# Kernel tuning notes

Hardware: AMD Instinct MI355X
Metric: run time of the kernel (lower is better)

Reference implementation:

```python
import jax, jax.numpy as jnp
import numpy as np

B, N, C, HF, NUM_CLASS = 2, 500, 512, 25, 20
POOL = 7
STRIDE = 32.0


def setup_inputs() -> dict:
    key = jax.random.key(0)
    ks = jax.random.split(key, 9)
    feature_map = jax.random.normal(ks[0], (B, C, HF, HF), dtype=jnp.float32)
    # Post-NMS boxes (r0, c0, r1, c1) in image coords [0, 800], guaranteed
    # to have floor(r1/32) - floor(r0/32) >= 1 so every crop is non-empty
    # (matches the module's assumption that extract_fature_map is non-empty).
    r0 = jax.random.uniform(ks[1], (B, N), minval=0.0, maxval=700.0)
    c0 = jax.random.uniform(ks[2], (B, N), minval=0.0, maxval=700.0)
    hh = jax.random.uniform(ks[3], (B, N), minval=64.0, maxval=100.0)
    ww = jax.random.uniform(ks[4], (B, N), minval=64.0, maxval=100.0)
    boxes = jnp.stack([r0, c0, jnp.clip(r0 + hh, 0, 800.0), jnp.clip(c0 + ww, 0, 800.0)], axis=-1)
    fc_w = jax.random.normal(ks[5], (4096, POOL * POOL * C), dtype=jnp.float32) * 0.01
    fc_b = jnp.zeros((4096,), dtype=jnp.float32)
    l_w = jax.random.normal(ks[6], (NUM_CLASS * 4, 4096), dtype=jnp.float32) * 0.01
    l_b = jnp.zeros((NUM_CLASS * 4,), dtype=jnp.float32)
    s_w = jax.random.normal(ks[7], (NUM_CLASS + 1, 4096), dtype=jnp.float32) * 0.01
    s_b = jnp.zeros((NUM_CLASS + 1,), dtype=jnp.float32)
    return {"feature_map": feature_map, "boxes": boxes, "fc_w": fc_w, "fc_b": fc_b,
            "l_w": l_w, "l_b": l_b, "s_w": s_w, "s_b": s_b}


def _bin_edges(start, size):
    # Adaptive avg pool bin boundaries: floor(k*size/P), ceil((k+1)*size/P),
    # offset by the crop start. start/size: [B, N] int32. Returns [B, N, P] each.
    k = jnp.arange(POOL, dtype=jnp.int32)
    lo = start[..., None] + (k * size[..., None]) // POOL
    hi = start[..., None] + ((k + 1) * size[..., None] + POOL - 1) // POOL
    return lo, hi


def _roi_pool(feature_map, boxes):
    # Exact equivalent of per-box crop + AdaptiveAvgPool2d((7,7)) via an
    # integral image, fully vectorized over all B*N boxes.
    coords = (boxes / STRIDE).astype(jnp.int32)  # int() cast, coords >= 0
    r0, c0, r1, c1 = coords[..., 0], coords[..., 1], coords[..., 2], coords[..., 3]
    rs, re = _bin_edges(r0, r1 - r0)  # [B, N, 7]
    cs, ce = _bin_edges(c0, c1 - c0)
    # Integral image: I[b, ch, i, j] = sum(fm[b, ch, :i, :j]); shape [B, C, 26, 26]
    I = jnp.pad(feature_map, ((0, 0), (0, 0), (1, 0), (1, 0))).cumsum(2).cumsum(3)

    def pool_one(I_b, rs_b, re_b, cs_b, ce_b):
        def corner(r, c):  # [N,7],[N,7] -> [C, N, 7, 7]
            return I_b[:, r[:, :, None], c[:, None, :]]
        S = corner(re_b, ce_b) - corner(rs_b, ce_b) - corner(re_b, cs_b) + corner(rs_b, cs_b)
        area = ((re_b - rs_b)[:, :, None] * (ce_b - cs_b)[:, None, :]).astype(I_b.dtype)
        return S / area  # [C, N, 7, 7]

    pooled = jax.vmap(pool_one)(I, rs, re, cs, ce)  # [B, C, N, 7, 7]
    # torch.flatten(pool, 0) flattens (C, 7, 7) in C-major order
    return pooled.transpose(0, 2, 1, 3, 4).reshape(B, N, C * POOL * POOL)


def reference(feature_map, boxes, fc_w, fc_b, l_w, l_b, s_w, s_b):
    feat = _roi_pool(feature_map, boxes)                      # [B, N, 25088]
    fc = jnp.einsum('bnk,fk->bnf', feat, fc_w) + fc_b         # [B, N, 4096]
    l_fc = jnp.einsum('bnf,lf->bnl', fc, l_w) + l_b           # [B, N, 80]
    s_fc = jnp.einsum('bnf,sf->bns', fc, s_w) + s_b           # [B, N, 21]
    max_index = jnp.argmax(s_fc, axis=-1)                     # [B, N]
    idx = max_index[..., None] + jnp.arange(4)                # l_fc[mi:mi+4]
    l_out = jnp.take_along_axis(l_fc, idx, axis=-1)           # [B, N, 4]
    return l_out, s_fc
```

## Files before the change

### kernel.cpp

```cpp
#include <hip/hip_runtime.h>

#define BATCH 2
#define NBOX 500
#define CH 512
#define HFD 25
#define IW 26
#define IRC 676
#define IRCP2 768
#define PPOOL 7
#define NP 49
#define NCLS 20
#define NO 101
#define OP2 112
#define MFRAG 7
#define KD 25088
#define FDIM 4096
#define NSTEP_TOT 128
#define FSPLIT 4
#define WCSTEPS 32
#define S_WC ((size_t)KD * OP2)
#define NFRAG_H (NP * 16 * MFRAG)

typedef __attribute__((ext_vector_type(4))) float f32x4;
typedef __attribute__((ext_vector_type(8))) short bf16x8;
typedef __attribute__((ext_vector_type(4))) unsigned int u32v4;

#define MFMA16 __builtin_amdgcn_mfma_f32_16x16x32_bf16

typedef __attribute__((address_space(1))) const unsigned int guint;
typedef __attribute__((address_space(3))) unsigned int luint;
#define GLL16(G, L) __builtin_amdgcn_global_load_lds((guint*)(G), (luint*)(L), 16, 0, 0)

#define SPLIT2PK(V0, V1, HW, MW)                                       \
  {                                                                    \
    unsigned u0_ = __float_as_uint(V0), u1_ = __float_as_uint(V1);     \
    HW = (u0_ >> 16) | (u1_ & 0xffff0000u);                            \
    float r0_ = (V0) - __uint_as_float(u0_ & 0xffff0000u);             \
    float r1_ = (V1) - __uint_as_float(u1_ & 0xffff0000u);             \
    unsigned m0_ = __float_as_uint(r0_), m1_ = __float_as_uint(r1_);   \
    m0_ += 0x7fffu + ((m0_ >> 16) & 1u);                               \
    m1_ += 0x7fffu + ((m1_ >> 16) & 1u);                               \
    MW = (m0_ >> 16) | (m1_ & 0xffff0000u);                            \
  }

#define SPLIT2T(V0, V1, HW, MW)                                        \
  {                                                                    \
    unsigned u0_ = __float_as_uint(V0), u1_ = __float_as_uint(V1);     \
    HW = (u0_ >> 16) | (u1_ & 0xffff0000u);                            \
    float r0_ = (V0) - __uint_as_float(u0_ & 0xffff0000u);             \
    float r1_ = (V1) - __uint_as_float(u1_ & 0xffff0000u);             \
    MW = (__float_as_uint(r0_) >> 16) |                                \
         (__float_as_uint(r1_) & 0xffff0000u);                         \
  }

#define SPLIT3PK(V0, V1, HW, MW, LW)                                   \
  {                                                                    \
    unsigned u0_ = __float_as_uint(V0), u1_ = __float_as_uint(V1);     \
    HW = (u0_ >> 16) | (u1_ & 0xffff0000u);                            \
    float r0_ = (V0) - __uint_as_float(u0_ & 0xffff0000u);             \
    float r1_ = (V1) - __uint_as_float(u1_ & 0xffff0000u);             \
    unsigned m0_ = __float_as_uint(r0_), m1_ = __float_as_uint(r1_);   \
    MW = (m0_ >> 16) | (m1_ & 0xffff0000u);                            \
    float s0_ = r0_ - __uint_as_float(m0_ & 0xffff0000u);              \
    float s1_ = r1_ - __uint_as_float(m1_ & 0xffff0000u);              \
    LW = (__float_as_uint(s0_) >> 16) |                                \
         (__float_as_uint(s1_) & 0xffff0000u);                         \
  }

__global__ void k_lt(const float* __restrict__ lw, const float* __restrict__ sw,
                     u32v4* __restrict__ Ahi, u32v4* __restrict__ Amd) {
    int t = blockIdx.x * 256 + threadIdx.x;
    if (t >= MFRAG * NSTEP_TOT * 64) return;
    int lane = t & 63;
    int wv = t >> 6;
    int s = wv & 127, mf = wv >> 7;
    int o = mf * 16 + (lane & 15);
    int f0 = s * 32 + (lane >> 4) * 8;
    float v[8];
    const float* row = nullptr;
    if (o < 80) row = lw + (size_t)o * FDIM;
    else if (o < NO) row = sw + (size_t)(o - 80) * FDIM;
    #pragma unroll
    for (int j = 0; j < 8; ++j) v[j] = row ? row[f0 + j] : 0.f;
    u32v4 hw, mw;
    #pragma unroll
    for (int w = 0; w < 4; ++w)
        SPLIT2PK(v[2 * w], v[2 * w + 1], hw[w], mw[w]);
    Ahi[(size_t)wv * 64 + lane] = hw;
    Amd[(size_t)wv * 64 + lane] = mw;
}

__global__ void k_integral(const float* __restrict__ fm, float* __restrict__ I) {
    int gtid = blockIdx.x * blockDim.x + threadIdx.x;
    int wid = gtid >> 6;
    int lane = gtid & 63;
    if (wid >= BATCH * CH) return;
    const float* src = fm + (size_t)wid * (HFD * HFD);
    float* dst = I + (size_t)wid * IRCP2;
    if (lane < IW) dst[lane] = 0.f;
    if (lane >= 1 && lane < IW) dst[lane * IW] = 0.f;
    int c = lane;
    float acc = 0.f;
    for (int r = 0; r < HFD; ++r) {
        float v = (c < HFD) ? src[r * HFD + c] : 0.f;
        #pragma unroll
        for (int d = 1; d < 32; d <<= 1) {
            float t = __shfl_up(v, d, 64);
            if (lane >= d) v += t;
        }
        acc += v;
        if (c < HFD) dst[(r + 1) * IW + (c + 1)] = acc;
    }
}

__global__ void k_bias(const float* __restrict__ lw, const float* __restrict__ sw,
                       const float* __restrict__ fcb, const float* __restrict__ lb,
                       const float* __restrict__ sb, float* __restrict__ bias) {
    int o = blockIdx.x;
    __shared__ float red[256];
    float s = 0.f;
    if (o < NO) {
        const float* row = (o < 80) ? (lw + (size_t)o * FDIM) : (sw + (size_t)(o - 80) * FDIM);
        for (int f = threadIdx.x; f < FDIM; f += 256) s += row[f] * fcb[f];
    }
    red[threadIdx.x] = s;
    __syncthreads();
    for (int st = 128; st > 0; st >>= 1) {
        if ((int)threadIdx.x < st) red[threadIdx.x] += red[threadIdx.x + st];
        __syncthreads();
    }
    if (threadIdx.x == 0) {
        float bv = 0.f;
        if (o < 80) bv = red[0] + lb[o];
        else if (o < NO) bv = red[0] + sb[o - 80];
        bias[o] = bv;
    }
}

#define WC_STAGE(S, DB)                                                       \
  {                                                                           \
    const float* gb_ = W1 + (size_t)(fs * 1024 + (S) * 32 + w) * KD + k0;     \
    _Pragma("unroll")                                                         \
    for (int i_ = 0; i_ < 8; ++i_) {                                          \
      unsigned gc_ = (lb16 ^ ((unsigned)(i_ >> 1) << 6)) >> 2;                \
      GLL16(gb_ + (size_t)(4 * i_) * KD + gc_,                                \
            &Bs[DB][i_ * 1024 + w * 256]);                                    \
    }                                                                         \
  }

#define WC_STEP(S, DB)                                                        \
  {                                                                           \
    u32v4 ah[MFRAG], am[MFRAG];                                               \
    _Pragma("unroll")                                                         \
    for (int mf = 0; mf < MFRAG; ++mf) {                                      \
      size_t ai = (size_t)((mf * 128 + fs * WCSTEPS + (S)) * 64 + lane);      \
      ah[mf] = Ahi[ai]; am[mf] = Amd[ai];                                     \
    }                                                                         \
    const char* bs_ = (const char*)&Bs[DB][0];                                \
    _Pragma("unroll")                                                         \
    for (int nf = 0; nf < 4; ++nf) {                                          \
      float bv[8];                                                            \
      _Pragma("unroll")                                                       \
      for (int j = 0; j < 8; ++j)                                             \
        bv[j] = *(const float*)(bs_ + (rowg * 8 + j) * 1024 + kb[nf]);        \
      u32v4 bhw, bmw;                                                         \
      _Pragma("unroll")                                                       \
      for (int w_ = 0; w_ < 4; ++w_)                                          \
        SPLIT2T(bv[2 * w_], bv[2 * w_ + 1], bhw[w_], bmw[w_]);                \
      bf16x8 bh = __builtin_bit_cast(bf16x8, bhw);                            \
      bf16x8 bm = __builtin_bit_cast(bf16x8, bmw);                            \
      _Pragma("unroll")                                                       \
      for (int mf = 0; mf < MFRAG; ++mf) {                                    \
        bf16x8 a_h = __builtin_bit_cast(bf16x8, ah[mf]);                      \
        bf16x8 a_m = __builtin_bit_cast(bf16x8, am[mf]);                      \
        acc[mf][nf] = MFMA16(a_h, bh, acc[mf][nf], 0, 0, 0);                  \
        acc[mf][nf] = MFMA16(a_m, bh, acc[mf][nf], 0, 0, 0);                  \
        acc[mf][nf] = MFMA16(a_h, bm, acc[mf][nf], 0, 0, 0);                  \
      }                                                                       \
    }                                                                         \
  }

__global__ void __launch_bounds__(256, 2) k_wc(const float* __restrict__ W1,
                                               const u32v4* __restrict__ Ahi,
                                               const u32v4* __restrict__ Amd,
                                               float* __restrict__ Wcp) {
    __shared__ float Bs[2][32 * 256];
    int lane = threadIdx.x & 63;
    int w = threadIdx.x >> 6;
    int kblk = blockIdx.x;
    int fs = blockIdx.y;
    int k0 = kblk * 256;
    int col = lane & 15, rowg = lane >> 4;
    unsigned lb16 = (unsigned)lane * 16;

    unsigned kb[4];
    #pragma unroll
    for (int nf = 0; nf < 4; ++nf)
        kb[nf] = ((unsigned)((w * 64 + nf * 16 + col) * 4)) ^ ((unsigned)rowg << 6);

    f32x4 acc[MFRAG][4];
    #pragma unroll
    for (int mf = 0; mf < MFRAG; ++mf)
        #pragma unroll
        for (int nf = 0; nf < 4; ++nf)
            acc[mf][nf] = (f32x4){0.f, 0.f, 0.f, 0.f};

    WC_STAGE(0, 0);
    __syncthreads();
    for (int s = 0; s < WCSTEPS; ++s) {
        int db = s & 1;
        if (s + 1 < WCSTEPS) WC_STAGE(s + 1, db ^ 1);
        WC_STEP(s, db);
        __syncthreads();
    }

    float* wp = Wcp + (size_t)fs * S_WC;
    #pragma unroll
    for (int mf = 0; mf < MFRAG; ++mf)
        #pragma unroll
        for (int nf = 0; nf < 4; ++nf) {
            size_t k = (size_t)k0 + w * 64 + nf * 16 + col;
            int o = mf * 16 + (rowg << 2);
            *(f32x4*)(wp + k * OP2 + o) = acc[mf][nf];
        }
}

__global__ void k_redsplit(const float* __restrict__ Wcp, u32v4* __restrict__ Whi,
                           u32v4* __restrict__ Wmd, u32v4* __restrict__ Wlo) {
    int t = blockIdx.x * 256 + threadIdx.x;
    int lane = t & 63;
    int fi = t >> 6;
    int p = fi / (16 * MFRAG);
    int rem = fi - p * (16 * MFRAG);
    int cs = rem / MFRAG, mf = rem - cs * MFRAG;
    int o = mf * 16 + (lane & 15);
    int c0 = cs * 32 + (lane >> 4) * 8;
    float v[8];
    #pragma unroll
    for (int j = 0; j < 8; ++j) {
        size_t base = ((size_t)(c0 + j) * NP + p) * OP2 + o;
        float s = 0.f;
        #pragma unroll
        for (int i = 0; i < FSPLIT; ++i) s += Wcp[base + (size_t)i * S_WC];
        v[j] = s;
    }
    u32v4 hw, mw, lww;
    #pragma unroll
    for (int w = 0; w < 4; ++w)
        SPLIT3PK(v[2 * w], v[2 * w + 1], hw[w], mw[w], lww[w]);
    Whi[(size_t)fi * 64 + lane] = hw;
    Wmd[(size_t)fi * 64 + lane] = mw;
    Wlo[(size_t)fi * 64 + lane] = lww;
}

#define KH_STEP(CUR, NXT, S)                                                  \
  {                                                                           \
    if ((S) + 1 < 16) {                                                       \
      _Pragma("unroll")                                                       \
      for (int nf = 0; nf < 2; ++nf)                                          \
        _Pragma("unroll")                                                     \
        for (int j = 0; j < 8; ++j)                                           \
          NXT[nf][j] = Ib[(size_t)(((S) + 1) * 32 + rowg * 8 + j) * IRCP2 + nf * 16]; \
    }                                                                         \
    bf16x8 bh[2], bm[2], bl[2];                                               \
    _Pragma("unroll")                                                         \
    for (int nf = 0; nf < 2; ++nf) {                                          \
      u32v4 bhw, bmw, blw;                                                    \
      _Pragma("unroll")                                                       \
      for (int w_ = 0; w_ < 4; ++w_)                                          \
        SPLIT3PK(CUR[nf][2 * w_], CUR[nf][2 * w_ + 1], bhw[w_], bmw[w_], blw[w_]); \
      bh[nf] = __builtin_bit_cast(bf16x8, bhw);                               \
      bm[nf] = __builtin_bit_cast(bf16x8, bmw);                               \
      bl[nf] = __builtin_bit_cast(bf16x8, blw);                               \
    }                                                                         \
    _Pragma("unroll")                                                         \
    for (int mf = 0; mf < MFRAG; ++mf) {                                      \
      size_t ai = (size_t)(((p * 16 + (S)) * MFRAG + mf) * 64 + lane);        \
      bf16x8 a_h = __builtin_bit_cast(bf16x8, Whi[ai]);                       \
      bf16x8 a_m = __builtin_bit_cast(bf16x8, Wmd[ai]);                       \
      bf16x8 a_l = __builtin_bit_cast(bf16x8, Wlo[ai]);                       \
      _Pragma("unroll")                                                       \
      for (int nf = 0; nf < 2; ++nf) {                                        \
        acc[mf][nf] = MFMA16(a_h, bh[nf], acc[mf][nf], 0, 0, 0);              \
        acc[mf][nf] = MFMA16(a_m, bh[nf], acc[mf][nf], 0, 0, 0);              \
        acc[mf][nf] = MFMA16(a_h, bm[nf], acc[mf][nf], 0, 0, 0);              \
        acc[mf][nf] = MFMA16(a_m, bm[nf], acc[mf][nf], 0, 0, 0);              \
        acc[mf][nf] = MFMA16(a_l, bh[nf], acc[mf][nf], 0, 0, 0);              \
        acc[mf][nf] = MFMA16(a_h, bl[nf], acc[mf][nf], 0, 0, 0);              \
      }                                                                       \
    }                                                                         \
  }

__global__ void __launch_bounds__(256, 2) k_h(const float* __restrict__ I,
                                              const u32v4* __restrict__ Whi,
                                              const u32v4* __restrict__ Wmd,
                                              const u32v4* __restrict__ Wlo,
                                              float* __restrict__ H) {
    int lane = threadIdx.x & 63;
    int w = threadIdx.x >> 6;
    int rcb = blockIdx.x, p = blockIdx.y, b = blockIdx.z;
    int col = lane & 15, rowg = lane >> 4;
    int rcw = rcb * 128 + w * 32;
    const float* Ib = I + (size_t)b * CH * IRCP2 + rcw + col;

    f32x4 acc[MFRAG][2];
    #pragma unroll
    for (int mf = 0; mf < MFRAG; ++mf) {
        acc[mf][0] = (f32x4){0.f, 0.f, 0.f, 0.f};
        acc[mf][1] = (f32x4){0.f, 0.f, 0.f, 0.f};
    }
    float ib0[2][8], ib1[2][8];
    #pragma unroll
    for (int nf = 0; nf < 2; ++nf)
        #pragma unroll
        for (int j = 0; j < 8; ++j)
            ib0[nf][j] = Ib[(size_t)(rowg * 8 + j) * IRCP2 + nf * 16];

    for (int s = 0; s < 16; s += 2) {
        KH_STEP(ib0, ib1, s);
        KH_STEP(ib1, ib0, s + 1);
    }

    #pragma unroll
    for (int mf = 0; mf < MFRAG; ++mf)
        #pragma unroll
        for (int nf = 0; nf < 2; ++nf) {
            int rc = rcw + nf * 16 + col;
            if (rc < IRC) {
                float* hp = H + (((size_t)(b * NP + p)) * IRC + rc) * OP2
                            + mf * 16 + rowg * 4;
                *(f32x4*)hp = acc[mf][nf];
            }
        }
}

__global__ void __launch_bounds__(512) k_out(const float* __restrict__ boxes,
                                             const float* __restrict__ H,
                                             const float* __restrict__ bias,
                                             float* __restrict__ out) {
    int n = blockIdx.x, b = blockIdx.y;
    int t = threadIdx.x;
    __shared__ int srs[PPOOL], sre[PPOOL], scs[PPOOL], sce[PPOOL];
    __shared__ float sinv[NP];
    __shared__ float psum[4][NO];
    __shared__ float sl[NO];
    __shared__ int smi;
    const float* bx = boxes + ((size_t)b * NBOX + n) * 4;
    if (t < PPOOL) {
        int r0 = (int)(bx[0] / 32.0f);
        int c0 = (int)(bx[1] / 32.0f);
        int r1 = (int)(bx[2] / 32.0f);
        int c1 = (int)(bx[3] / 32.0f);
        int sr = r1 - r0, sc = c1 - c0;
        srs[t] = r0 + (t * sr) / PPOOL;
        sre[t] = r0 + ((t + 1) * sr + PPOOL - 1) / PPOOL;
        scs[t] = c0 + (t * sc) / PPOOL;
        sce[t] = c0 + ((t + 1) * sc + PPOOL - 1) / PPOOL;
    }
    __syncthreads();
    if (t < NP) {
        int ph = t / PPOOL, pw = t - ph * PPOOL;
        sinv[t] = 1.0f / (float)((sre[ph] - srs[ph]) * (sce[pw] - scs[pw]));
    }
    __syncthreads();
    int o = t & 127, q = t >> 7;
    if (o < NO) {
        int p0 = q ? (12 * q + 1) : 0;
        int p1 = 12 * q + 13;
        float acc = 0.f;
        const float* Hb = H + (size_t)b * NP * IRC * OP2 + o;
        for (int p = p0; p < p1; ++p) {
            int ph = p / PPOOL, pw = p - ph * PPOOL;
            const float* Hp = Hb + (size_t)p * IRC * OP2;
            int re = sre[ph], rs = srs[ph], ce = sce[pw], cs = scs[pw];
            float v = Hp[(size_t)(re * IW + ce) * OP2] - Hp[(size_t)(rs * IW + ce) * OP2]
                    - Hp[(size_t)(re * IW + cs) * OP2] + Hp[(size_t)(rs * IW + cs) * OP2];
            acc += v * sinv[p];
        }
        psum[q][o] = acc;
    }
    __syncthreads();
    if (t < NO) {
        float v = psum[0][t] + psum[1][t] + psum[2][t] + psum[3][t] + bias[t];
        sl[t] = v;
        if (t >= 80)
            out[(size_t)(4 * BATCH * NBOX) + ((size_t)b * NBOX + n) * (NCLS + 1) + (t - 80)] = v;
    }
    __syncthreads();
    if (t == 0) {
        float best = sl[80]; int mi = 0;
        for (int s = 1; s <= NCLS; ++s) {
            float v = sl[80 + s];
            if (v > best) { best = v; mi = s; }
        }
        smi = mi;
    }
    __syncthreads();
    if (t < 4) out[((size_t)b * NBOX + n) * 4 + t] = sl[smi + t];
}

extern "C" void kernel_launch(void* const* d_in, const int* in_sizes, int n_in,
                              void* d_out, int out_size, void* d_ws, size_t ws_size,
                              hipStream_t stream) {
    const float* fm    = (const float*)d_in[0];
    const float* boxes = (const float*)d_in[1];
    const float* fcw   = (const float*)d_in[2];
    const float* fcb   = (const float*)d_in[3];
    const float* lw    = (const float*)d_in[4];
    const float* lb    = (const float*)d_in[5];
    const float* sw    = (const float*)d_in[6];
    const float* sb    = (const float*)d_in[7];
    float* out = (float*)d_out;

    float* ws = (float*)d_ws;
    float* I    = ws;
    u32v4* Ahi  = (u32v4*)(I + (size_t)BATCH * CH * IRCP2);
    u32v4* Amd  = Ahi + MFRAG * NSTEP_TOT * 64;
    float* bias = (float*)(Amd + MFRAG * NSTEP_TOT * 64);
    float* Wcp  = bias + 128;
    u32v4* Whi  = (u32v4*)(Wcp + (size_t)FSPLIT * S_WC);
    u32v4* Wmd  = Whi + (size_t)NFRAG_H * 64;
    u32v4* Wlo  = Wmd + (size_t)NFRAG_H * 64;
    float* H    = (float*)(Wlo + (size_t)NFRAG_H * 64);

    hipLaunchKernelGGL(k_lt, dim3(224), dim3(256), 0, stream, lw, sw, Ahi, Amd);
    hipLaunchKernelGGL(k_integral, dim3(256), dim3(256), 0, stream, fm, I);
    hipLaunchKernelGGL(k_bias, dim3(104), dim3(256), 0, stream, lw, sw, fcb, lb, sb, bias);
    hipLaunchKernelGGL(k_wc, dim3(98, FSPLIT), dim3(256), 0, stream, fcw, Ahi, Amd, Wcp);
    hipLaunchKernelGGL(k_redsplit, dim3(NFRAG_H * 64 / 256), dim3(256), 0, stream, Wcp, Whi, Wmd, Wlo);
    hipLaunchKernelGGL(k_h, dim3(6, NP, BATCH), dim3(256), 0, stream, I, Whi, Wmd, Wlo, H);
    hipLaunchKernelGGL(k_out, dim3(NBOX, BATCH), dim3(512), 0, stream, boxes, H, bias, out);
}
```

Before: 234.1 us.

## Pre-split integral image to transposed bf16 planes and stage weights via LDS

The integral image is now written transposed (rc-major, channel-minor) and already split into three bf16 planes inside k_integral, so k_h loads B fragments as contiguous 16-byte vectors instead of doing strided scalar loads and per-step splitting. Weight fragments for each k-step are staged into double-buffered shared memory with global_load_lds, with a barrier per step. This is meant to cut global load count and ALU splitting work in the main MFMA kernel. In exchange it adds a full-workspace memset, scattered 2-byte stores in k_integral, and 43KB of LDS per block, which may limit occupancy.

```diff
diff --git a/kernel.cpp b/kernel.cpp
--- a/kernel.cpp
+++ b/kernel.cpp
@@ -6,7 +6,7 @@
 #define HFD 25
 #define IW 26
 #define IRC 676
-#define IRCP2 768
+#define ITROWS 768
 #define PPOOL 7
 #define NP 49
 #define NCLS 20
@@ -20,6 +20,7 @@
 #define WCSTEPS 32
 #define S_WC ((size_t)KD * OP2)
 #define NFRAG_H (NP * 16 * MFRAG)
+#define ITSZ ((size_t)BATCH * ITROWS * CH)
 
 typedef __attribute__((ext_vector_type(4))) float f32x4;
 typedef __attribute__((ext_vector_type(8))) short bf16x8;
@@ -90,15 +91,14 @@
     Amd[(size_t)wv * 64 + lane] = mw;
 }
 
-__global__ void k_integral(const float* __restrict__ fm, float* __restrict__ I) {
+__global__ void k_integral(const float* __restrict__ fm, ushort* __restrict__ IThi,
+                           ushort* __restrict__ ITmd, ushort* __restrict__ ITlo) {
     int gtid = blockIdx.x * blockDim.x + threadIdx.x;
     int wid = gtid >> 6;
     int lane = gtid & 63;
     if (wid >= BATCH * CH) return;
+    int b = wid / CH, ch = wid - b * CH;
     const float* src = fm + (size_t)wid * (HFD * HFD);
-    float* dst = I + (size_t)wid * IRCP2;
-    if (lane < IW) dst[lane] = 0.f;
-    if (lane >= 1 && lane < IW) dst[lane * IW] = 0.f;
     int c = lane;
     float acc = 0.f;
     for (int r = 0; r < HFD; ++r) {
@@ -109,7 +109,17 @@
             if (lane >= d) v += t;
         }
         acc += v;
-        if (c < HFD) dst[(r + 1) * IW + (c + 1)] = acc;
+        if (c < HFD) {
+            int rc = (r + 1) * IW + (c + 1);
+            size_t base = ((size_t)b * ITROWS + rc) * CH + ch;
+            unsigned u = __float_as_uint(acc);
+            float r1 = acc - __uint_as_float(u & 0xffff0000u);
+            unsigned um = __float_as_uint(r1);
+            float r2 = r1 - __uint_as_float(um & 0xffff0000u);
+            IThi[base] = (ushort)(u >> 16);
+            ITmd[base] = (ushort)(um >> 16);
+            ITlo[base] = (ushort)(__float_as_uint(r2) >> 16);
+        }
     }
 }
 
@@ -253,32 +263,35 @@
     Wlo[(size_t)fi * 64 + lane] = lww;
 }
 
-#define KH_STEP(CUR, NXT, S)                                                  \
+#define KH_STAGE(S, DB)                                                       \
   {                                                                           \
-    if ((S) + 1 < 16) {                                                       \
-      _Pragma("unroll")                                                       \
-      for (int nf = 0; nf < 2; ++nf)                                          \
-        _Pragma("unroll")                                                     \
-        for (int j = 0; j < 8; ++j)                                           \
-          NXT[nf][j] = Ib[(size_t)(((S) + 1) * 32 + rowg * 8 + j) * IRCP2 + nf * 16]; \
-    }                                                                         \
+    size_t so_ = (size_t)(p * 16 + (S)) * 448;                                \
+    GLL16(Whi + so_ + t, &Ws[DB][t]);                                         \
+    GLL16(Wmd + so_ + t, &Ws[DB][448 + t]);                                   \
+    GLL16(Wlo + so_ + t, &Ws[DB][896 + t]);                                   \
+    if (t < 192) {                                                            \
+      GLL16(Whi + so_ + 256 + t, &Ws[DB][256 + t]);                           \
+      GLL16(Wmd + so_ + 256 + t, &Ws[DB][704 + t]);                           \
+      GLL16(Wlo + so_ + 256 + t, &Ws[DB][1152 + t]);                          \
+    }                                                                         \
+  }
+
+#define KH_STEP(S, DB)                                                        \
+  {                                                                           \
     bf16x8 bh[2], bm[2], bl[2];                                               \
     _Pragma("unroll")                                                         \
     for (int nf = 0; nf < 2; ++nf) {                                          \
-      u32v4 bhw, bmw, blw;                                                    \
-      _Pragma("unroll")                                                       \
-      for (int w_ = 0; w_ < 4; ++w_)                                          \
-        SPLIT3PK(CUR[nf][2 * w_], CUR[nf][2 * w_ + 1], bhw[w_], bmw[w_], blw[w_]); \
-      bh[nf] = __builtin_bit_cast(bf16x8, bhw);                               \
-      bm[nf] = __builtin_bit_cast(bf16x8, bmw);                               \
-      bl[nf] = __builtin_bit_cast(bf16x8, blw);                               \
+      size_t ib = ((size_t)b * ITROWS + rcw + nf * 16 + col) * CH             \
+                  + (S) * 32 + rowg * 8;                                      \
+      bh[nf] = __builtin_bit_cast(bf16x8, *(const u32v4*)(IThi + ib));        \
+      bm[nf] = __builtin_bit_cast(bf16x8, *(const u32v4*)(ITmd + ib));        \
+      bl[nf] = __builtin_bit_cast(bf16x8, *(const u32v4*)(ITlo + ib));        \
     }                                                                         \
     _Pragma("unroll")                                                         \
     for (int mf = 0; mf < MFRAG; ++mf) {                                      \
-      size_t ai = (size_t)(((p * 16 + (S)) * MFRAG + mf) * 64 + lane);        \
-      bf16x8 a_h = __builtin_bit_cast(bf16x8, Whi[ai]);                       \
-      bf16x8 a_m = __builtin_bit_cast(bf16x8, Wmd[ai]);                       \
-      bf16x8 a_l = __builtin_bit_cast(bf16x8, Wlo[ai]);                       \
+      bf16x8 a_h = __builtin_bit_cast(bf16x8, Ws[DB][mf * 64 + lane]);        \
+      bf16x8 a_m = __builtin_bit_cast(bf16x8, Ws[DB][448 + mf * 64 + lane]);  \
+      bf16x8 a_l = __builtin_bit_cast(bf16x8, Ws[DB][896 + mf * 64 + lane]);  \
       _Pragma("unroll")                                                       \
       for (int nf = 0; nf < 2; ++nf) {                                        \
         acc[mf][nf] = MFMA16(a_h, bh[nf], acc[mf][nf], 0, 0, 0);              \
@@ -291,17 +304,20 @@
     }                                                                         \
   }
 
-__global__ void __launch_bounds__(256, 2) k_h(const float* __restrict__ I,
+__global__ void __launch_bounds__(256, 2) k_h(const ushort* __restrict__ IThi,
+                                              const ushort* __restrict__ ITmd,
+                                              const ushort* __restrict__ ITlo,
                                               const u32v4* __restrict__ Whi,
                                               const u32v4* __restrict__ Wmd,
                                               const u32v4* __restrict__ Wlo,
                                               float* __restrict__ H) {
-    int lane = threadIdx.x & 63;
-    int w = threadIdx.x >> 6;
+    __shared__ u32v4 Ws[2][1344];
+    int t = threadIdx.x;
+    int lane = t & 63;
+    int w = t >> 6;
     int rcb = blockIdx.x, p = blockIdx.y, b = blockIdx.z;
     int col = lane & 15, rowg = lane >> 4;
     int rcw = rcb * 128 + w * 32;
-    const float* Ib = I + (size_t)b * CH * IRCP2 + rcw + col;
 
     f32x4 acc[MFRAG][2];
     #pragma unroll
@@ -309,16 +325,14 @@
         acc[mf][0] = (f32x4){0.f, 0.f, 0.f, 0.f};
         acc[mf][1] = (f32x4){0.f, 0.f, 0.f, 0.f};
     }
-    float ib0[2][8], ib1[2][8];
-    #pragma unroll
-    for (int nf = 0; nf < 2; ++nf)
-        #pragma unroll
-        for (int j = 0; j < 8; ++j)
-            ib0[nf][j] = Ib[(size_t)(rowg * 8 + j) * IRCP2 + nf * 16];
-
-    for (int s = 0; s < 16; s += 2) {
-        KH_STEP(ib0, ib1, s);
-        KH_STEP(ib1, ib0, s + 1);
+
+    KH_STAGE(0, 0);
+    __syncthreads();
+    for (int s = 0; s < 16; ++s) {
+        int db = s & 1;
+        if (s + 1 < 16) KH_STAGE(s + 1, db ^ 1);
+        KH_STEP(s, db);
+        __syncthreads();
     }
 
     #pragma unroll
@@ -412,9 +426,11 @@
     const float* sb    = (const float*)d_in[7];
     float* out = (float*)d_out;
 
-    float* ws = (float*)d_ws;
-    float* I    = ws;
-    u32v4* Ahi  = (u32v4*)(I + (size_t)BATCH * CH * IRCP2);
+    char* ws = (char*)d_ws;
+    ushort* IThi = (ushort*)ws;
+    ushort* ITmd = IThi + ITSZ;
+    ushort* ITlo = ITmd + ITSZ;
+    u32v4* Ahi  = (u32v4*)(ITlo + ITSZ);
     u32v4* Amd  = Ahi + MFRAG * NSTEP_TOT * 64;
     float* bias = (float*)(Amd + MFRAG * NSTEP_TOT * 64);
     float* Wcp  = bias + 128;
@@ -423,11 +439,12 @@
     u32v4* Wlo  = Wmd + (size_t)NFRAG_H * 64;
     float* H    = (float*)(Wlo + (size_t)NFRAG_H * 64);
 
+    hipMemsetAsync(IThi, 0, 3 * ITSZ * sizeof(ushort), stream);
     hipLaunchKernelGGL(k_lt, dim3(224), dim3(256), 0, stream, lw, sw, Ahi, Amd);
-    hipLaunchKernelGGL(k_integral, dim3(256), dim3(256), 0, stream, fm, I);
+    hipLaunchKernelGGL(k_integral, dim3(256), dim3(256), 0, stream, fm, IThi, ITmd, ITlo);
     hipLaunchKernelGGL(k_bias, dim3(104), dim3(256), 0, stream, lw, sw, fcb, lb, sb, bias);
     hipLaunchKernelGGL(k_wc, dim3(98, FSPLIT), dim3(256), 0, stream, fcw, Ahi, Amd, Wcp);
     hipLaunchKernelGGL(k_redsplit, dim3(NFRAG_H * 64 / 256), dim3(256), 0, stream, Wcp, Whi, Wmd, Wlo);
-    hipLaunchKernelGGL(k_h, dim3(6, NP, BATCH), dim3(256), 0, stream, I, Whi, Wmd, Wlo, H);
+    hipLaunchKernelGGL(k_h, dim3(6, NP, BATCH), dim3(256), 0, stream, IThi, ITmd, ITlo, Whi, Wmd, Wlo, H);
     hipLaunchKernelGGL(k_out, dim3(NBOX, BATCH), dim3(512), 0, stream, boxes, H, bias, out);
 }
```

Measured after the change: 241.0 us. 1.03x slower.
